# Optimization experiments

Measured on AMD Instinct MI355X. Metric: run time of the kernel, lower is better.

Reference implementation:

```python
import jax, jax.numpy as jnp
import numpy as np

B, N, C, H = 4, 2048, 1024, 16
HD = C // H  # head_dim = 64


def setup_inputs() -> dict:
    key = jax.random.key(0)
    ks = jax.random.split(key, 16)
    s = 0.02
    return {
        "x": jax.random.normal(ks[0], (B, N, C), dtype=jnp.float32),
        # qkv_proj: Linear(C, 3C): weight (3C, C), bias (3C,)
        "W_qkv": jax.random.normal(ks[1], (3 * C, C), dtype=jnp.float32) * s,
        "b_qkv": jax.random.normal(ks[2], (3 * C,), dtype=jnp.float32) * s,
        # out_proj: Linear(C, C)
        "W_out": jax.random.normal(ks[3], (C, C), dtype=jnp.float32) * s,
        "b_out": jax.random.normal(ks[4], (C,), dtype=jnp.float32) * s,
        # dynamically-reassigned position bias: shape (1, N, H, H) per the code's
        # (B, num_heads=N, seq_len=H, seq_len=H) score tensor
        "pos_bias": jax.random.normal(ks[5], (1, N, H, H), dtype=jnp.float32) * 0.01,
        # conv_proj: Linear(C, C)
        "W_cp": jax.random.normal(ks[6], (C, C), dtype=jnp.float32) * s,
        "b_cp": jax.random.normal(ks[7], (C,), dtype=jnp.float32) * s,
        # pointwise Conv1d(C, C, k=1): weight (C, C) after squeezing kernel dim
        "W_pw": jax.random.normal(ks[8], (C, C), dtype=jnp.float32) * s,
        "b_pw": jax.random.normal(ks[9], (C,), dtype=jnp.float32) * s,
        # depthwise Conv1d(C, C, k=3, groups=C): weight (C, 3)
        "W_dw": jax.random.normal(ks[10], (C, 3), dtype=jnp.float32) * s,
        "b_dw": jax.random.normal(ks[11], (C,), dtype=jnp.float32) * s,
        # token_wise_proj: Linear(C, C)
        "W_tw": jax.random.normal(ks[12], (C, C), dtype=jnp.float32) * s,
        "b_tw": jax.random.normal(ks[13], (C,), dtype=jnp.float32) * s,
    }


def reference(x, W_qkv, b_qkv, W_out, b_out, pos_bias, W_cp, b_cp,
              W_pw, b_pw, W_dw, b_dw, W_tw, b_tw) -> jnp.ndarray:
    Bx, Nx, Cx = x.shape
    scale = HD ** -0.5
    # qkv -> (B, N, H, 3*HD), chunk into q,k,v of (B, N, H, HD).
    # NOTE: faithful to the torch code, heads stay on axis 2; the matmul
    # contracts head_dim giving (B, N, H, H) scores (attention over heads).
    qkv = (x @ W_qkv.T + b_qkv).reshape(Bx, Nx, H, 3 * HD)
    q, k, v = jnp.split(qkv, 3, axis=-1)
    scores = jnp.einsum('bnhd,bngd->bnhg', q, k) * scale + pos_bias
    attn = jax.nn.softmax(scores, axis=-1)
    attn_out = jnp.einsum('bnhg,bngd->bnhd', attn, v).reshape(Bx, Nx, Cx)
    attn_out = attn_out @ W_out.T + b_out

    # Convolutional branch
    xc = x @ W_cp.T + b_cp          # conv_proj
    xc = xc @ W_pw.T + b_pw          # pointwise conv (k=1) == linear over channels
    xp = jnp.pad(xc, ((0, 0), (1, 1), (0, 0)))  # pad seq for k=3, padding=1
    xc = (xp[:, :-2] * W_dw[:, 0] + xp[:, 1:-1] * W_dw[:, 1]
          + xp[:, 2:] * W_dw[:, 2] + b_dw)      # depthwise conv
    xc = xc @ W_tw.T + b_tw          # token_wise_proj

    return attn_out + xc
```

## Files before the change

kernel.cpp:

```cpp
#include <hip/hip_runtime.h>
#include <hip/hip_bf16.h>
#include <stdint.h>

typedef __bf16 bf16_t;
typedef __attribute__((ext_vector_type(8))) __bf16 bf16x8;
typedef __attribute__((ext_vector_type(4))) __bf16 bf16x4;
typedef __attribute__((ext_vector_type(4))) float floatx4;
typedef __attribute__((ext_vector_type(4))) _Float16 half4_t;

#define GLDS16(g, l)                                                          \
  __builtin_amdgcn_global_load_lds(                                           \
      (const __attribute__((address_space(1))) void*)(g),                     \
      (__attribute__((address_space(3))) void*)(l), 16, 0, 0)

template <int IT, int JT, typename OT>
__global__ __launch_bounds__(256) void gemm_bt(
    const bf16_t* __restrict__ A, const bf16_t* __restrict__ B,
    const float* __restrict__ bias, OT* __restrict__ C, int M, int N, int K) {
  constexpr int AROWS = 32 * IT;
  constexpr int BROWS = 32 * JT;
  constexpr int COLS = BROWS;
  constexpr int STAGE = (AROWS + BROWS) * 64;
  constexpr int EPI = (sizeof(OT) == 2) ? AROWS * COLS : 0;
  constexpr int SME = STAGE > EPI ? STAGE : EPI;
  __shared__ bf16_t sm[SME];
  bf16_t* As = sm;
  bf16_t* Bs = sm + AROWS * 64;

  const int tid = threadIdx.x;
  const int wave = tid >> 6;
  const int lane = tid & 63;
  const int quad = lane >> 4;
  const int l16 = lane & 15;
  const int m0 = blockIdx.x * AROWS;
  const int n0 = blockIdx.y * BROWS;
  const int wm = (wave >> 1) * (IT * 16);
  const int wn = (wave & 1) * (JT * 16);

  const int ra = wave * (8 * IT) + (lane >> 3);
  const int ga = ((lane & 7) ^ (ra & 7)) * 8;
  const int rb = wave * (8 * JT) + (lane >> 3);
  const int gb = ((lane & 7) ^ (rb & 7)) * 8;
  const bf16_t* Ab = A + (size_t)(m0 + ra) * K + ga;
  const bf16_t* Bb = B + (size_t)(n0 + rb) * K + gb;
  const int p0 = (quad ^ (l16 & 7)) * 8;

  floatx4 acc[IT][JT];
  const floatx4 zf = {0.f, 0.f, 0.f, 0.f};
#pragma unroll
  for (int i = 0; i < IT; ++i)
#pragma unroll
    for (int j = 0; j < JT; ++j) acc[i][j] = zf;

  for (int k0 = 0; k0 < K; k0 += 64) {
#pragma unroll
    for (int t = 0; t < IT; ++t)
      GLDS16(Ab + (size_t)(t * 8) * K + k0, As + (wave * (64 * IT) + t * 64) * 8);
#pragma unroll
    for (int t = 0; t < JT; ++t)
      GLDS16(Bb + (size_t)(t * 8) * K + k0, Bs + (wave * (64 * JT) + t * 64) * 8);
    __syncthreads();
#pragma unroll
    for (int ks = 0; ks < 2; ++ks) {
      const int ko = p0 ^ (ks * 32);
      bf16x8 af[IT], bfr[JT];
#pragma unroll
      for (int i = 0; i < IT; ++i)
        af[i] = *(const bf16x8*)(As + (wm + i * 16 + l16) * 64 + ko);
#pragma unroll
      for (int j = 0; j < JT; ++j)
        bfr[j] = *(const bf16x8*)(Bs + (wn + j * 16 + l16) * 64 + ko);
#pragma unroll
      for (int i = 0; i < IT; ++i)
#pragma unroll
        for (int j = 0; j < JT; ++j)
          acc[i][j] = __builtin_amdgcn_mfma_f32_16x16x32_bf16(
              bfr[j], af[i], acc[i][j], 0, 0, 0);
    }
    __syncthreads();
  }

  if constexpr (sizeof(OT) == 4) {
#pragma unroll
    for (int j = 0; j < JT; ++j) {
      const int colb = n0 + wn + j * 16 + quad * 4;
      floatx4 bv = zf;
      if (bias) bv = *(const floatx4*)(bias + colb);
#pragma unroll
      for (int i = 0; i < IT; ++i) {
        const int row = m0 + wm + i * 16 + l16;
        floatx4 v = acc[i][j] + bv;
        *(floatx4*)((float*)C + (size_t)row * N + colb) = v;
      }
    }
  } else {
    constexpr int SWZ = COLS / 32;
    constexpr int CPR = COLS / 8;
    constexpr int PASSES = (AROWS * CPR) / 256;
#pragma unroll
    for (int j = 0; j < JT; ++j) {
      const int colb = n0 + wn + j * 16 + quad * 4;
      floatx4 bv = zf;
      if (bias) bv = *(const floatx4*)(bias + colb);
      const int gcol = (wn + j * 16 + quad * 4) >> 2;
#pragma unroll
      for (int i = 0; i < IT; ++i) {
        const int rl = wm + i * 16 + l16;
        floatx4 v = acc[i][j] + bv;
        union {
          bf16_t b[4];
          uint2 u2;
        } pk;
        pk.b[0] = (bf16_t)v[0];
        pk.b[1] = (bf16_t)v[1];
        pk.b[2] = (bf16_t)v[2];
        pk.b[3] = (bf16_t)v[3];
        const int gsw = gcol ^ ((rl & 7) * SWZ);
        *(uint2*)(sm + rl * COLS + gsw * 4) = pk.u2;
      }
    }
    __syncthreads();
    bf16_t* Cb = (bf16_t*)C;
#pragma unroll
    for (int pass = 0; pass < PASSES; ++pass) {
      const int f = pass * 256 + tid;
      const int row = f / CPR;
      const int c16 = f % CPR;
      const int g0 = (2 * c16) ^ ((row & 7) * SWZ);
      uint4 v = *(const uint4*)(sm + row * COLS + g0 * 4);
      *(uint4*)(Cb + (size_t)(m0 + row) * N + n0 + c16 * 8) = v;
    }
  }
}

__global__ __launch_bounds__(256) void prep2_k(
    const float* __restrict__ x, bf16_t* __restrict__ x_bf,
    const float* __restrict__ Wqkv, bf16_t* __restrict__ Wbig1,
    const float* __restrict__ Wpw, bf16_t* __restrict__ Wpw_bf,
    const float* __restrict__ Wout, const float* __restrict__ Wtw,
    bf16_t* __restrict__ Wbig2, const float* __restrict__ bqkv,
    float* __restrict__ bias1, const float* __restrict__ bout,
    const float* __restrict__ btw, float* __restrict__ bias2,
    const float* __restrict__ Wcp, bf16_t* __restrict__ WcpT,
    const float* __restrict__ bcp, const float* __restrict__ bpw) {
  __shared__ float t[32][33];
  const int b = blockIdx.x, tid = threadIdx.x;
  auto cvt4 = [](const float* in, bf16_t* out, int i) {
    floatx4 v = ((const floatx4*)in)[i];
    bf16x4 o;
    o[0] = (bf16_t)v[0];
    o[1] = (bf16_t)v[1];
    o[2] = (bf16_t)v[2];
    o[3] = (bf16_t)v[3];
    ((bf16x4*)out)[i] = o;
  };
  if (b < 8192) {
    cvt4(x, x_bf, b * 256 + tid);
  } else if (b < 11264) {
    cvt4(Wqkv, Wbig1, (b - 8192) * 256 + tid);
  } else if (b < 12288) {
    cvt4(Wpw, Wpw_bf, (b - 11264) * 256 + tid);
  } else if (b < 14336) {
    const bool second = b >= 13312;
    int i = (b - (second ? 13312 : 12288)) * 256 + tid;
    floatx4 v = ((const floatx4*)(second ? Wtw : Wout))[i];
    bf16x4 o;
    o[0] = (bf16_t)v[0];
    o[1] = (bf16_t)v[1];
    o[2] = (bf16_t)v[2];
    o[3] = (bf16_t)v[3];
    int row = i >> 8, c4 = i & 255;
    *(bf16x4*)(Wbig2 + (size_t)row * 2048 + (second ? 1024 : 0) + c4 * 4) = o;
  } else if (b < 14339) {
    int i = (b - 14336) * 256 + tid;
    if (i < 768) ((floatx4*)bias1)[i] = ((const floatx4*)bqkv)[i];
  } else if (b == 14339) {
    ((floatx4*)bias2)[tid] =
        ((const floatx4*)bout)[tid] + ((const floatx4*)btw)[tid];
  } else if (b < 15364) {
    const int tb = b - 14340;
    const int bx = (tb & 31) * 32, by = (tb >> 5) * 32;
    const int tx = tid & 31, ty = tid >> 5;
#pragma unroll
    for (int iq = 0; iq < 4; ++iq)
      t[ty + iq * 8][tx] = Wcp[(size_t)(by + ty + iq * 8) * 1024 + bx + tx];
    __syncthreads();
#pragma unroll
    for (int iq = 0; iq < 4; ++iq)
      WcpT[(size_t)(bx + ty + iq * 8) * 1024 + by + tx] =
          (bf16_t)t[tx][ty + iq * 8];
  } else {
    const int row = (b - 15364) * 4 + (tid >> 6);
    const int l = tid & 63;
    const float* wr = Wpw + (size_t)row * 1024;
    float s = 0.f;
    for (int j = l; j < 1024; j += 64) s += wr[j] * bcp[j];
#pragma unroll
    for (int o = 32; o > 0; o >>= 1) s += __shfl_down(s, o);
    if (l == 0) bias1[3072 + row] = s + bpw[row];
  }
}

static __device__ inline void exp8(uint32_t w0, uint32_t w1, uint32_t w2,
                                   uint32_t w3, float* f) {
  f[0] = __uint_as_float(w0 << 16);
  f[1] = __uint_as_float(w0 & 0xffff0000u);
  f[2] = __uint_as_float(w1 << 16);
  f[3] = __uint_as_float(w1 & 0xffff0000u);
  f[4] = __uint_as_float(w2 << 16);
  f[5] = __uint_as_float(w2 & 0xffff0000u);
  f[6] = __uint_as_float(w3 << 16);
  f[7] = __uint_as_float(w3 & 0xffff0000u);
}

__global__ __launch_bounds__(256) void mid_k(const bf16_t* __restrict__ G1,
                                             const float* __restrict__ pos,
                                             const float* __restrict__ Wdw,
                                             const float* __restrict__ bdw,
                                             bf16_t* __restrict__ Mid) {
  __shared__ bf16_t ost[4][16 * 68];
  const int tid = threadIdx.x;
  if (blockIdx.x < 2048) {
    const int wave = tid >> 6, lane = tid & 63;
    const int p = blockIdx.x * 4 + wave;
    const int l16 = lane & 15, quad = lane >> 4;
    const bf16_t* row = G1 + (size_t)p * 4096;
    const bf16_t* qb = row + l16 * 192 + quad * 8;

    bf16x8 q0 = *(const bf16x8*)(qb);
    bf16x8 q1 = *(const bf16x8*)(qb + 32);
    bf16x8 k0 = *(const bf16x8*)(qb + 64);
    bf16x8 k1 = *(const bf16x8*)(qb + 96);
    floatx4 S = {0.f, 0.f, 0.f, 0.f};
    S = __builtin_amdgcn_mfma_f32_16x16x32_bf16(k0, q0, S, 0, 0, 0);
    S = __builtin_amdgcn_mfma_f32_16x16x32_bf16(k1, q1, S, 0, 0, 0);

    const floatx4 pb = *(const floatx4*)(pos + (size_t)(p & 2047) * 256 +
                                         l16 * 16 + quad * 4);
    float v[4];
#pragma unroll
    for (int r = 0; r < 4; ++r) v[r] = S[r] * 0.125f + pb[r];

    float m = fmaxf(fmaxf(v[0], v[1]), fmaxf(v[2], v[3]));
    m = fmaxf(m, __shfl_xor(m, 16));
    m = fmaxf(m, __shfl_xor(m, 32));
    float e[4], sum = 0.f;
#pragma unroll
    for (int r = 0; r < 4; ++r) {
      e[r] = __expf(v[r] - m);
      sum += e[r];
    }
    sum += __shfl_xor(sum, 16);
    sum += __shfl_xor(sum, 32);
    const float inv = 1.0f / sum;
    half4_t pa;
#pragma unroll
    for (int r = 0; r < 4; ++r) pa[r] = (_Float16)(e[r] * inv);

    const bf16_t* vb_base = row + 128 + l16;
    const floatx4 zf = {0.f, 0.f, 0.f, 0.f};
    floatx4 o[4];
#pragma unroll
    for (int t = 0; t < 4; ++t) {
      half4_t vb;
#pragma unroll
      for (int j = 0; j < 4; ++j)
        vb[j] = (_Float16)(float)vb_base[(quad * 4 + j) * 192 + t * 16];
      o[t] = __builtin_amdgcn_mfma_f32_16x16x16f16(pa, vb, zf, 0, 0, 0);
    }

    bf16_t* ow = ost[wave];
#pragma unroll
    for (int r = 0; r < 4; ++r)
#pragma unroll
      for (int t = 0; t < 4; ++t)
        ow[(quad * 4 + r) * 68 + t * 16 + l16] = (bf16_t)o[t][r];
    const int h2 = lane >> 2, m4 = lane & 3;
    const bf16_t* srcp = ow + h2 * 68 + m4 * 16;
    uint2 a0 = *(const uint2*)(srcp);
    uint2 a1 = *(const uint2*)(srcp + 4);
    uint2 a2 = *(const uint2*)(srcp + 8);
    uint2 a3 = *(const uint2*)(srcp + 12);
    uint4 s0 = {a0.x, a0.y, a1.x, a1.y};
    uint4 s1 = {a2.x, a2.y, a3.x, a3.y};
    uint4* dst = (uint4*)(Mid + (size_t)p * 2048 + h2 * 64 + m4 * 16);
    dst[0] = s0;
    dst[1] = s1;
  } else {
    const bf16_t* in = G1 + 3072;
    bf16_t* out = Mid + 1024;
    const int item = (blockIdx.x - 2048) * 256 + tid;
    const int cc = item & 127, rowg = item >> 7;
    const int c0 = cc * 8;
    float w0[8], w1[8], w2[8], bb[8];
#pragma unroll
    for (int c = 0; c < 8; ++c) {
      w0[c] = Wdw[(c0 + c) * 3];
      w1[c] = Wdw[(c0 + c) * 3 + 1];
      w2[c] = Wdw[(c0 + c) * 3 + 2];
      bb[c] = bdw[c0 + c];
    }
#pragma unroll
    for (int jr = 0; jr < 4; ++jr) {
      const int tt = rowg * 4 + jr;
      const int n = tt & 2047;
      const bf16_t* ip = in + (size_t)tt * 4096 + c0;
      const uint4 z4 = {0, 0, 0, 0};
      uint4 um = (n > 0) ? *(const uint4*)(ip - 4096) : z4;
      uint4 uc = *(const uint4*)(ip);
      uint4 up = (n < 2047) ? *(const uint4*)(ip + 4096) : z4;
      float fm[8], fc[8], fp[8];
      exp8(um.x, um.y, um.z, um.w, fm);
      exp8(uc.x, uc.y, uc.z, uc.w, fc);
      exp8(up.x, up.y, up.z, up.w, fp);
      union {
        bf16_t b[8];
        uint4 u;
      } pk;
#pragma unroll
      for (int c = 0; c < 8; ++c)
        pk.b[c] =
            (bf16_t)(bb[c] + fm[c] * w0[c] + fc[c] * w1[c] + fp[c] * w2[c]);
      *(uint4*)(out + (size_t)tt * 2048 + c0) = pk.u;
    }
  }
}

extern "C" void kernel_launch(void* const* d_in, const int* in_sizes, int n_in,
                              void* d_out, int out_size, void* d_ws,
                              size_t ws_size, hipStream_t stream) {
  (void)in_sizes; (void)n_in; (void)out_size; (void)ws_size;
  const float* x = (const float*)d_in[0];
  const float* Wqkv = (const float*)d_in[1];
  const float* bqkv = (const float*)d_in[2];
  const float* Wout = (const float*)d_in[3];
  const float* bout = (const float*)d_in[4];
  const float* pos = (const float*)d_in[5];
  const float* Wcp = (const float*)d_in[6];
  const float* bcp = (const float*)d_in[7];
  const float* Wpw = (const float*)d_in[8];
  const float* bpw = (const float*)d_in[9];
  const float* Wdw = (const float*)d_in[10];
  const float* bdw = (const float*)d_in[11];
  const float* Wtw = (const float*)d_in[12];
  const float* btw = (const float*)d_in[13];
  float* out = (float*)d_out;

  char* ws = (char*)d_ws;
  const size_t MB = 1024ull * 1024ull;
  bf16_t* x_bf = (bf16_t*)(ws + 0);
  bf16_t* Wbig1 = (bf16_t*)(ws + 16 * MB);
  bf16_t* WcpT = (bf16_t*)(ws + 24 * MB);
  bf16_t* Wpw_bf = (bf16_t*)(ws + 26 * MB);
  bf16_t* Mid = (bf16_t*)(ws + 0);
  bf16_t* Wbig2 = (bf16_t*)(ws + 32 * MB);
  float* bias1 = (float*)(ws + 36 * MB);
  float* bias2 = (float*)(ws + 36 * MB + 65536);
  bf16_t* G1out = (bf16_t*)(ws + 37 * MB);

  prep2_k<<<15620, 256, 0, stream>>>(x, x_bf, Wqkv, Wbig1, Wpw, Wpw_bf, Wout,
                                     Wtw, Wbig2, bqkv, bias1, bout, btw, bias2,
                                     Wcp, WcpT, bcp, bpw);

  gemm_bt<2, 2, bf16_t><<<dim3(16, 16), 256, 0, stream>>>(
      Wpw_bf, WcpT, nullptr, Wbig1 + (size_t)3072 * 1024, 1024, 1024, 1024);

  gemm_bt<4, 4, bf16_t><<<dim3(64, 32), 256, 0, stream>>>(
      x_bf, Wbig1, bias1, G1out, 8192, 4096, 1024);

  mid_k<<<3072, 256, 0, stream>>>(G1out, pos, Wdw, bdw, Mid);

  gemm_bt<4, 4, float><<<dim3(64, 8), 256, 0, stream>>>(Mid, Wbig2, bias2,
                                                        out, 8192, 1024, 2048);
}
```

Before: 273.9 us.

## Replace main QKV GEMM with 256x256-tile 8-wave pipelined kernel

Adds a new bf16 GEMM kernel with 256x256 output tiles, 512 threads (8 waves) and a double-buffered LDS pipeline. It interleaves direct global-to-LDS loads with MFMA blocks, using explicit barriers, vmcnt waits and setprio, plus an XCD-aware block swizzle. It replaces the 128x128 gemm_bt for the large x·Wbig1 projection. The goal is higher MFMA utilisation and more operand reuse, at the cost of 128KB of LDS per block and a schedule that is hand-tuned and fragile.

New measurement: 276.8 us. About the same (+1.0%).

```diff
diff --git a/kernel.cpp b/kernel.cpp
--- a/kernel.cpp
+++ b/kernel.cpp
@@ -131,6 +131,160 @@
       *(uint4*)(Cb + (size_t)(m0 + row) * N + n0 + c16 * 8) = v;
     }
   }
+}
+
+#define BAR8 asm volatile("s_barrier" ::: "memory")
+#define VMCNT(n) asm volatile("s_waitcnt vmcnt(" #n ")" ::: "memory")
+
+__global__ __launch_bounds__(512, 2) void gemm8p(
+    const bf16_t* __restrict__ A, const bf16_t* __restrict__ B,
+    const float* __restrict__ bias, bf16_t* __restrict__ C, int M, int N,
+    int K) {
+  __shared__ bf16_t sm8[65536];
+  bf16_t* As = sm8;
+  bf16_t* Bs = sm8 + 32768;
+
+  const int tid = threadIdx.x;
+  const int wave = tid >> 6, lane = tid & 63;
+  const int l16 = lane & 15, quad = lane >> 4;
+  const int wm = (wave >> 2) * 128, wn = (wave & 3) * 64;
+
+  const int lin = blockIdx.y * gridDim.x + blockIdx.x;
+  const int nwg = gridDim.x * gridDim.y;
+  const int chunk = nwg >> 3;
+  const int swz = (lin & 7) * chunk + (lin >> 3);
+  const int bm = swz / gridDim.x;
+  const int bn = swz % gridDim.x;
+  const int m0 = bm << 8, n0 = bn << 8;
+
+  const int srow = wave * 32 + (lane >> 2);
+  const int kswz = ((lane & 3) * 8) ^ ((lane >> 5) << 4);
+  const bf16_t* Ag = A + (size_t)(m0 + srow) * K + kswz;
+  const bf16_t* Bg = B + (size_t)(n0 + srow) * K + kswz;
+  const int sdst = wave * 1024;
+  const size_t a16k = (size_t)K << 4;
+
+  const int koe = (quad * 8) ^ ((l16 & 8) << 1);
+  const int aoff = (wm + l16) * 32 + koe;
+  const int boff = (wn + l16) * 32 + koe;
+
+  floatx4 acc[8][4];
+  const floatx4 zf = {0.f, 0.f, 0.f, 0.f};
+#pragma unroll
+  for (int i = 0; i < 8; ++i)
+#pragma unroll
+    for (int j = 0; j < 4; ++j) acc[i][j] = zf;
+
+  bf16x8 af[4], bfr[4];
+
+#define STG_A(buf, kh, TOFF)                                     \
+  do {                                                           \
+    bf16_t* _d = As + (buf)*16384 + (kh)*8192 + sdst;            \
+    GLDS16(Ag + (TOFF) + (kh)*32, _d);                           \
+    GLDS16(Ag + a16k + (TOFF) + (kh)*32, _d + 512);              \
+  } while (0)
+#define STG_B(buf, kh, TOFF)                                     \
+  do {                                                           \
+    bf16_t* _d = Bs + (buf)*16384 + (kh)*8192 + sdst;            \
+    GLDS16(Bg + (TOFF) + (kh)*32, _d);                           \
+    GLDS16(Bg + a16k + (TOFF) + (kh)*32, _d + 512);              \
+  } while (0)
+#define LDA4(buf, ks, mb)                                        \
+  do {                                                           \
+    const bf16_t* _p = As + (buf)*16384 + (ks)*8192 + aoff + (mb)*512; \
+    af[0] = *(const bf16x8*)(_p);                                \
+    af[1] = *(const bf16x8*)(_p + 512);                          \
+    af[2] = *(const bf16x8*)(_p + 1024);                         \
+    af[3] = *(const bf16x8*)(_p + 1536);                         \
+  } while (0)
+#define LDB4(buf, ks)                                            \
+  do {                                                           \
+    const bf16_t* _p = Bs + (buf)*16384 + (ks)*8192 + boff;      \
+    bfr[0] = *(const bf16x8*)(_p);                               \
+    bfr[1] = *(const bf16x8*)(_p + 512);                         \
+    bfr[2] = *(const bf16x8*)(_p + 1024);                        \
+    bfr[3] = *(const bf16x8*)(_p + 1536);                        \
+  } while (0)
+#define MFMA16(mb)                                               \
+  do {                                                           \
+    __builtin_amdgcn_s_setprio(1);                               \
+    _Pragma("unroll") for (int _i = 0; _i < 4; ++_i)             \
+        _Pragma("unroll") for (int _j = 0; _j < 4; ++_j)         \
+            acc[(mb) + _i][_j] =                                 \
+                __builtin_amdgcn_mfma_f32_16x16x32_bf16(         \
+                    bfr[_j], af[_i], acc[(mb) + _i][_j], 0, 0, 0); \
+    __builtin_amdgcn_s_setprio(0);                               \
+  } while (0)
+
+  STG_A(0, 0, 0);
+  STG_A(0, 1, 0);
+  STG_B(0, 0, 0);
+  STG_B(0, 1, 0);
+  STG_B(1, 0, 64);
+  STG_A(1, 0, 64);
+  STG_B(1, 1, 64);
+  VMCNT(6);
+  BAR8;
+
+  const int NT = K >> 6;
+  for (int it = 0; it < NT / 2 - 1; ++it) {
+    LDA4(0, 0, 0); LDB4(0, 0); STG_A(1, 1, 64);            BAR8; MFMA16(0); BAR8;
+    LDA4(0, 0, 4);             STG_B(0, 0, 128);           BAR8; MFMA16(4); BAR8;
+    LDA4(0, 1, 0); LDB4(0, 1); STG_A(0, 0, 128);           BAR8; MFMA16(0); BAR8;
+    LDA4(0, 1, 4);             STG_B(0, 1, 128); VMCNT(6); BAR8; MFMA16(4); BAR8;
+    LDA4(1, 0, 0); LDB4(1, 0); STG_A(0, 1, 128);           BAR8; MFMA16(0); BAR8;
+    LDA4(1, 0, 4);             STG_B(1, 0, 192);           BAR8; MFMA16(4); BAR8;
+    LDA4(1, 1, 0); LDB4(1, 1); STG_A(1, 0, 192);           BAR8; MFMA16(0); BAR8;
+    LDA4(1, 1, 4);             STG_B(1, 1, 192); VMCNT(6); BAR8; MFMA16(4); BAR8;
+    Ag += 128;
+    Bg += 128;
+  }
+  LDA4(0, 0, 0); LDB4(0, 0); STG_A(1, 1, 64); BAR8; MFMA16(0); BAR8;
+  LDA4(0, 0, 4);                              BAR8; MFMA16(4); BAR8;
+  LDA4(0, 1, 0); LDB4(0, 1);                  BAR8; MFMA16(0); BAR8;
+  LDA4(0, 1, 4);             VMCNT(0);        BAR8; MFMA16(4); BAR8;
+  LDA4(1, 0, 0); LDB4(1, 0);                  BAR8; MFMA16(0); BAR8;
+  LDA4(1, 0, 4);                              BAR8; MFMA16(4); BAR8;
+  LDA4(1, 1, 0); LDB4(1, 1);                  BAR8; MFMA16(0); BAR8;
+  LDA4(1, 1, 4);                              BAR8; MFMA16(4); BAR8;
+
+  const int crow_b = wm + l16;
+#pragma unroll
+  for (int nj = 0; nj < 4; ++nj) {
+    const int colb = wn + nj * 16 + quad * 4;
+    floatx4 bv = zf;
+    if (bias) bv = *(const floatx4*)(bias + n0 + colb);
+#pragma unroll
+    for (int mi = 0; mi < 8; ++mi) {
+      const int row = crow_b + mi * 16;
+      floatx4 v = acc[mi][nj] + bv;
+      union {
+        bf16_t b[4];
+        uint2 u2;
+      } pk;
+      pk.b[0] = (bf16_t)v[0];
+      pk.b[1] = (bf16_t)v[1];
+      pk.b[2] = (bf16_t)v[2];
+      pk.b[3] = (bf16_t)v[3];
+      const int cb = (colb * 2) ^ ((row & 31) << 4);
+      *(uint2*)((char*)sm8 + row * 512 + cb) = pk.u2;
+    }
+  }
+  __syncthreads();
+#pragma unroll
+  for (int pass = 0; pass < 16; ++pass) {
+    const int flat = pass * 8192 + tid * 16;
+    const int row = flat >> 9;
+    const int cb = flat & 511;
+    const int cbs = cb ^ ((row & 31) << 4);
+    uint4 v = *(const uint4*)((char*)sm8 + row * 512 + cbs);
+    *(uint4*)((char*)C + ((size_t)(m0 + row) * N + n0) * 2 + cb) = v;
+  }
+#undef STG_A
+#undef STG_B
+#undef LDA4
+#undef LDB4
+#undef MFMA16
 }
 
 __global__ __launch_bounds__(256) void prep2_k(
@@ -365,8 +519,8 @@
   gemm_bt<2, 2, bf16_t><<<dim3(16, 16), 256, 0, stream>>>(
       Wpw_bf, WcpT, nullptr, Wbig1 + (size_t)3072 * 1024, 1024, 1024, 1024);
 
-  gemm_bt<4, 4, bf16_t><<<dim3(64, 32), 256, 0, stream>>>(
-      x_bf, Wbig1, bias1, G1out, 8192, 4096, 1024);
+  gemm8p<<<dim3(16, 32), 512, 0, stream>>>(x_bf, Wbig1, bias1, G1out, 8192,
+                                           4096, 1024);
 
   mid_k<<<3072, 256, 0, stream>>>(G1out, pos, Wdw, bdw, Mid);
 
```
